# Performance work log

Hardware: AMD Instinct MI355X
Metric: run time of the kernel (lower is better)

The kernel has to match this reference:

```python
import jax, jax.numpy as jnp
import numpy as np

B, D, F, H = 4096, 1024, 1024, 8


def setup_inputs() -> dict:
    key = jax.random.key(0)
    k1, k2, k3, k4 = jax.random.split(key, 4)
    inputs = jax.random.normal(k1, (B, D), dtype=jnp.float32)
    indices = jax.random.randint(k2, (B,), 0, H, dtype=jnp.int64)
    # lecun_normal-like scale for kernel; zeros bias per flax defaults, but use
    # small random bias so gradients are nontrivial
    kernel = jax.random.normal(k3, (H, D, F), dtype=jnp.float32) / np.sqrt(D)
    bias = jax.random.normal(k4, (H, F), dtype=jnp.float32) * 0.01
    return {"inputs": inputs, "indices": indices, "kernel": kernel, "bias": bias}


def reference(inputs, indices, kernel, bias):
    # Original: per-example gather of kernel[idx] ([D,F]) then x[idx] @ w + b.
    # Equivalent math, vectorized: compute all heads densely then select the
    # routed head per example (avoids materializing a [B,D,F] gathered tensor).
    y = jnp.einsum("bd,hdf->bhf", inputs, kernel) + bias[None, :, :]  # [B,H,F]
    return y[jnp.arange(inputs.shape[0]), indices]  # [B,F]
```

## Files before the change

kernel.cpp:

```cpp
#include <hip/hip_runtime.h>


typedef __attribute__((ext_vector_type(8))) short bf16x8;
typedef __attribute__((ext_vector_type(4))) float f32x4;

#define WAITV(N) asm volatile("s_waitcnt vmcnt(" #N ")" ::: "memory")

static __device__ __forceinline__ unsigned short f2bf(float f) {
  union { float f; unsigned int u; } c; c.f = f;
  unsigned int u = c.u;
  return (unsigned short)((u + 0x7fffu + ((u >> 16) & 1u)) >> 16);
}

static __device__ __forceinline__ void gload16(const void* g, void* s) {
  __builtin_amdgcn_global_load_lds(
      (const __attribute__((address_space(1))) void*)g,
      (__attribute__((address_space(3))) void*)s, 16, 0, 0);
}

__global__ __launch_bounds__(256) void k_prep(
    const float* __restrict__ W, const int* __restrict__ idx,
    unsigned short* __restrict__ Wt, int* __restrict__ cnt,
    int* __restrict__ base8, int* __restrict__ rows) {
  const int bid = blockIdx.x;
  const int t = threadIdx.x;

  if (bid >= 2048) {
    __shared__ int sc[256][8];
    int myi[16];
#pragma unroll
    for (int i = 0; i < 4; ++i) {
      const int4 v = *(const int4*)(idx + t * 16 + i * 4);
      myi[i * 4 + 0] = v.x; myi[i * 4 + 1] = v.y;
      myi[i * 4 + 2] = v.z; myi[i * 4 + 3] = v.w;
    }
    int c[8];
#pragma unroll
    for (int h = 0; h < 8; ++h) c[h] = 0;
#pragma unroll
    for (int e = 0; e < 16; ++e)
#pragma unroll
      for (int h = 0; h < 8; ++h) c[h] += (myi[e] == h) ? 1 : 0;

    int val[8];
#pragma unroll
    for (int h = 0; h < 8; ++h) { val[h] = c[h]; sc[t][h] = c[h]; }
    __syncthreads();
    for (int off = 1; off < 256; off <<= 1) {
      int nb[8];
#pragma unroll
      for (int h = 0; h < 8; ++h) nb[h] = (t >= off) ? sc[t - off][h] : 0;
      __syncthreads();
#pragma unroll
      for (int h = 0; h < 8; ++h) { val[h] += nb[h]; sc[t][h] = val[h]; }
      __syncthreads();
    }
    int tot[8], excl[8];
#pragma unroll
    for (int h = 0; h < 8; ++h) tot[h] = sc[255][h];
#pragma unroll
    for (int h = 0; h < 8; ++h) excl[h] = val[h] - c[h];
    int bases[9];
    bases[0] = 0;
#pragma unroll
    for (int h = 0; h < 7; ++h) bases[h + 1] = (bases[h] + tot[h] + 7) & ~7;
    bases[8] = bases[7] + tot[7];
#pragma unroll
    for (int h = 0; h < 8; ++h) {
      int pos = bases[h] + excl[h];
#pragma unroll
      for (int e = 0; e < 16; ++e) {
        if (myi[e] == h) { rows[pos] = t * 16 + e; ++pos; }
      }
    }
    if (t < 56) {
      const int hh = t >> 3, j = t & 7;
      const int pos = bases[hh] + tot[hh] + j;
      if (pos < bases[hh + 1]) rows[pos] = 0;
    }
    if (t < 128) {
      const int pos = bases[8] + t;
      if (pos < 4160) rows[pos] = 0;
    }
    if (t < 8) cnt[t] = tot[t];
    if (t == 0) {
#pragma unroll
      for (int h = 0; h < 9; ++h) base8[h] = bases[h];
    }
    return;
  }

  __shared__ unsigned short tile[64][68];
  const int h = bid >> 8;
  const int rem = bid & 255;
  const int d0 = (rem >> 4) << 6;
  const int f0 = (rem & 15) << 6;
  const int c4 = (t & 15) * 4;
  const int r0 = t >> 4;
#pragma unroll
  for (int i = 0; i < 4; ++i) {
    const int r = r0 + i * 16;
    const float4 v = *(const float4*)(W + (size_t)(h * 1024 + d0 + r) * 1024 + f0 + c4);
    tile[r][c4 + 0] = f2bf(v.x);
    tile[r][c4 + 1] = f2bf(v.y);
    tile[r][c4 + 2] = f2bf(v.z);
    tile[r][c4 + 3] = f2bf(v.w);
  }
  __syncthreads();
  const int chunk = c4 >> 3;
  const int half = (c4 >> 2) & 1;
#pragma unroll
  for (int i = 0; i < 4; ++i) {
    const int fr = r0 + i * 16;
    const int frow = f0 + fr;
    ushort4 o;
    o.x = tile[c4 + 0][fr];
    o.y = tile[c4 + 1][fr];
    o.z = tile[c4 + 2][fr];
    o.w = tile[c4 + 3][fr];
    const int cS = chunk ^ (frow & 7);
    *(ushort4*)((char*)Wt + (size_t)(h * 1024 + frow) * 2048 +
                (d0 << 1) + (cS << 4) + (half << 3)) = o;
  }
}

__global__ __launch_bounds__(256) void k_gather(
    const float* __restrict__ X, const int* __restrict__ rows,
    unsigned short* __restrict__ Ap) {
  const int slot = blockIdx.x;
  const int b = rows[slot];
  const int t = threadIdx.x;
  const float4 v = *(const float4*)(X + (size_t)b * 1024 + t * 4);
  ushort4 o;
  o.x = f2bf(v.x); o.y = f2bf(v.y); o.z = f2bf(v.z); o.w = f2bf(v.w);
  const int g = t >> 4;
  const int cS = ((t >> 1) & 7) ^ (slot & 7);
  *(ushort4*)((char*)Ap + (size_t)slot * 2048 + (g << 7) + (cS << 4) +
              ((t & 1) << 3)) = o;
}

__global__ __launch_bounds__(256) void k_gemm(
    const unsigned short* __restrict__ Ap, const unsigned short* __restrict__ Wt,
    const int* __restrict__ rows, const int* __restrict__ cnt,
    const int* __restrict__ base8,
    const float* __restrict__ bias, float* __restrict__ out) {
  __shared__ __align__(16) unsigned short As[3][64 * 64];
  __shared__ __align__(16) unsigned short Bs[3][64 * 64];

  const int blk = blockIdx.x;
  const int h = blk & 7;
  const int nt = (blk >> 3) & 15;
  const int mt = blk >> 7;

  const int cnt_h = cnt[h];
  const int basep = base8[h];
  const int m0 = mt * 64;
  if (m0 >= cnt_h) return;
  const int n0 = nt * 64;

  const int t = threadIdx.x;
  const int lane = t & 63;
  const int wave = t >> 6;
  const int wr = wave >> 1, wc = wave & 1;

  const int srow = t >> 3;
  const int scol = (t & 7) << 4;
  int ar0 = basep + m0 + srow;      ar0 = ar0 < 4159 ? ar0 : 4159;
  int ar1 = basep + m0 + 32 + srow; ar1 = ar1 < 4159 ? ar1 : 4159;
  const char* aRow0 = (const char*)Ap + (size_t)ar0 * 2048 + scol;
  const char* aRow1 = (const char*)Ap + (size_t)ar1 * 2048 + scol;
  const char* bRow0 = (const char*)Wt + (size_t)(h * 1024 + n0 + srow) * 2048 + scol;
  const char* bRow1 = (const char*)Wt + (size_t)(h * 1024 + n0 + 32 + srow) * 2048 + scol;

  f32x4 acc[2][2];
#pragma unroll
  for (int m = 0; m < 2; ++m)
#pragma unroll
    for (int n = 0; n < 2; ++n)
      acc[m][n] = (f32x4){0.f, 0.f, 0.f, 0.f};

  auto stage = [&](char* aDst, char* bDst, int k0) {
    const int kby = k0 * 2;
    gload16(aRow0 + kby, aDst + t * 16);
    gload16(aRow1 + kby, aDst + 4096 + t * 16);
    gload16(bRow0 + kby, bDst + t * 16);
    gload16(bRow1 + kby, bDst + 4096 + t * 16);
  };

  const int swz = (lane & 7) << 4;
  const int ra = (wr * 32 + (lane & 15)) * 128;
  const int rb = (wc * 32 + (lane & 15)) * 128;
  const int kc = (lane >> 4) << 4;

  auto compute = [&](const char* ab, const char* bb) {
#pragma unroll
    for (int ksub = 0; ksub < 2; ++ksub) {
      const int co = ((ksub * 64) + kc) ^ swz;
      const bf16x8 a0 = *(const bf16x8*)(ab + ra + co);
      const bf16x8 a1 = *(const bf16x8*)(ab + ra + 2048 + co);
      const bf16x8 b0 = *(const bf16x8*)(bb + rb + co);
      const bf16x8 b1 = *(const bf16x8*)(bb + rb + 2048 + co);
      acc[0][0] = __builtin_amdgcn_mfma_f32_16x16x32_bf16(a0, b0, acc[0][0], 0, 0, 0);
      acc[0][1] = __builtin_amdgcn_mfma_f32_16x16x32_bf16(a0, b1, acc[0][1], 0, 0, 0);
      acc[1][0] = __builtin_amdgcn_mfma_f32_16x16x32_bf16(a1, b0, acc[1][0], 0, 0, 0);
      acc[1][1] = __builtin_amdgcn_mfma_f32_16x16x32_bf16(a1, b1, acc[1][1], 0, 0, 0);
    }
  };

  char* a0p = (char*)&As[0][0]; char* a1p = (char*)&As[1][0]; char* a2p = (char*)&As[2][0];
  char* b0p = (char*)&Bs[0][0]; char* b1p = (char*)&Bs[1][0]; char* b2p = (char*)&Bs[2][0];

  stage(a0p, b0p, 0);
  stage(a1p, b1p, 64);

  for (int ts = 0; ts < 15; ++ts) {
    WAITV(4);
    __builtin_amdgcn_s_barrier();
    __builtin_amdgcn_sched_barrier(0);
    if (ts < 14) stage(a2p, b2p, (ts + 2) * 64);
    __builtin_amdgcn_sched_barrier(0);
    compute(a0p, b0p);
    char* tA = a0p; a0p = a1p; a1p = a2p; a2p = tA;
    char* tB = b0p; b0p = b1p; b1p = b2p; b2p = tB;
  }
  WAITV(0);
  __builtin_amdgcn_s_barrier();
  __builtin_amdgcn_sched_barrier(0);
  compute(a0p, b0p);

  int rmap[2][4];
  bool vld[2][4];
#pragma unroll
  for (int m = 0; m < 2; ++m) {
#pragma unroll
    for (int j = 0; j < 4; ++j) {
      const int lr = wr * 32 + m * 16 + (lane >> 4) * 4 + j;
      const bool v = (m0 + lr) < cnt_h;
      vld[m][j] = v;
      rmap[m][j] = v ? rows[basep + m0 + lr] : 0;
    }
  }
#pragma unroll
  for (int n = 0; n < 2; ++n) {
    const int c = n0 + wc * 32 + n * 16 + (lane & 15);
    const float bv = bias[h * 1024 + c];
#pragma unroll
    for (int m = 0; m < 2; ++m) {
#pragma unroll
      for (int j = 0; j < 4; ++j) {
        if (vld[m][j])
          out[(size_t)rmap[m][j] * 1024 + c] = acc[m][n][j] + bv;
      }
    }
  }
}

extern "C" void kernel_launch(void* const* d_in, const int* in_sizes, int n_in,
                              void* d_out, int out_size, void* d_ws, size_t ws_size,
                              hipStream_t stream) {
  const float* X = (const float*)d_in[0];
  const int* idx = (const int*)d_in[1];
  const float* W = (const float*)d_in[2];
  const float* bias = (const float*)d_in[3];
  float* out = (float*)d_out;

  char* ws = (char*)d_ws;
  int* cnt = (int*)ws;
  int* base8 = (int*)(ws + 64);
  int* rows = (int*)(ws + 256);
  unsigned short* Wt = (unsigned short*)(ws + 32768);
  unsigned short* Ap = (unsigned short*)(ws + 32768 + 16777216);

  k_prep<<<dim3(2049), 256, 0, stream>>>(W, idx, Wt, cnt, base8, rows);
  k_gather<<<dim3(4160), 256, 0, stream>>>(X, rows, Ap);
  k_gemm<<<dim3(8 * 16 * 16), 256, 0, stream>>>(Ap, Wt, rows, cnt, base8, bias, out);
}
```

Before: 48.90 us.

## Pre-pack weights in MFMA fragment order and load B directly to registers

The prep kernel now writes the bf16 weights in a fragment-major layout, so each lane of a wave can load its MFMA B operand with one contiguous 16-byte global load. The GEMM stops staging B through LDS: it register-double-buffers B and keeps only a double-buffered A tile in shared memory. The goal is to cut LDS traffic and footprint and shorten the pipeline. The cost is higher register pressure and less latency hiding, since B now waits on a direct global load each step. Head segments are padded to 16 rows, which enlarges the gather grid and the zero-fill of the row list.

```diff
diff --git a/kernel.cpp b/kernel.cpp
--- a/kernel.cpp
+++ b/kernel.cpp
@@ -21,7 +21,7 @@
 __global__ __launch_bounds__(256) void k_prep(
     const float* __restrict__ W, const int* __restrict__ idx,
     unsigned short* __restrict__ Wt, int* __restrict__ cnt,
-    int* __restrict__ base8, int* __restrict__ rows) {
+    int* __restrict__ base16, int* __restrict__ rows) {
   const int bid = blockIdx.x;
   const int t = threadIdx.x;
 
@@ -63,7 +63,7 @@
     int bases[9];
     bases[0] = 0;
 #pragma unroll
-    for (int h = 0; h < 7; ++h) bases[h + 1] = (bases[h] + tot[h] + 7) & ~7;
+    for (int h = 0; h < 7; ++h) bases[h + 1] = (bases[h] + tot[h] + 15) & ~15;
     bases[8] = bases[7] + tot[7];
 #pragma unroll
     for (int h = 0; h < 8; ++h) {
@@ -73,54 +73,61 @@
         if (myi[e] == h) { rows[pos] = t * 16 + e; ++pos; }
       }
     }
-    if (t < 56) {
-      const int hh = t >> 3, j = t & 7;
+    if (t < 128) {
+      const int hh = t >> 4, j = t & 15;
       const int pos = bases[hh] + tot[hh] + j;
       if (pos < bases[hh + 1]) rows[pos] = 0;
     }
-    if (t < 128) {
+    {
       const int pos = bases[8] + t;
-      if (pos < 4160) rows[pos] = 0;
+      if (pos < 4352) rows[pos] = 0;
     }
     if (t < 8) cnt[t] = tot[t];
     if (t == 0) {
 #pragma unroll
-      for (int h = 0; h < 9; ++h) base8[h] = bases[h];
+      for (int h = 0; h < 9; ++h) base16[h] = bases[h];
     }
     return;
   }
 
-  __shared__ unsigned short tile[64][68];
+  __shared__ unsigned short tile[64][65];
   const int h = bid >> 8;
   const int rem = bid & 255;
   const int d0 = (rem >> 4) << 6;
   const int f0 = (rem & 15) << 6;
-  const int c4 = (t & 15) * 4;
-  const int r0 = t >> 4;
-#pragma unroll
-  for (int i = 0; i < 4; ++i) {
-    const int r = r0 + i * 16;
-    const float4 v = *(const float4*)(W + (size_t)(h * 1024 + d0 + r) * 1024 + f0 + c4);
-    tile[r][c4 + 0] = f2bf(v.x);
-    tile[r][c4 + 1] = f2bf(v.y);
-    tile[r][c4 + 2] = f2bf(v.z);
-    tile[r][c4 + 3] = f2bf(v.w);
+  {
+    const int c4 = (t & 15) * 4;
+    const int r0 = t >> 4;
+#pragma unroll
+    for (int i = 0; i < 4; ++i) {
+      const int r = r0 + i * 16;
+      const float4 v = *(const float4*)(W + (size_t)(h * 1024 + d0 + r) * 1024 + f0 + c4);
+      tile[r][c4 + 0] = f2bf(v.x);
+      tile[r][c4 + 1] = f2bf(v.y);
+      tile[r][c4 + 2] = f2bf(v.z);
+      tile[r][c4 + 3] = f2bf(v.w);
+    }
   }
   __syncthreads();
-  const int chunk = c4 >> 3;
-  const int half = (c4 >> 2) & 1;
-#pragma unroll
-  for (int i = 0; i < 4; ++i) {
-    const int fr = r0 + i * 16;
-    const int frow = f0 + fr;
+  const int fgl = t >> 6;
+  const int fr = t & 15;
+  const int ksl = (t >> 4) & 3;
+  const int frow = f0 + fgl * 16 + fr;
+  const int fg = frow >> 4;
+  const int kc = (d0 >> 5) + (ksl >> 1);
+  const int kg0 = (ksl & 1) * 2;
+  const size_t baseB = (((size_t)(h * 64 + fg) * 32) + kc) * 1024;
+#pragma unroll
+  for (int q = 0; q < 4; ++q) {
+    const int kg = kg0 + (q >> 1);
+    const int e = (q & 1) * 4;
+    const int dl = ksl * 16 + (q >> 1) * 8 + e;
     ushort4 o;
-    o.x = tile[c4 + 0][fr];
-    o.y = tile[c4 + 1][fr];
-    o.z = tile[c4 + 2][fr];
-    o.w = tile[c4 + 3][fr];
-    const int cS = chunk ^ (frow & 7);
-    *(ushort4*)((char*)Wt + (size_t)(h * 1024 + frow) * 2048 +
-                (d0 << 1) + (cS << 4) + (half << 3)) = o;
+    o.x = tile[dl + 0][fgl * 16 + fr];
+    o.y = tile[dl + 1][fgl * 16 + fr];
+    o.z = tile[dl + 2][fgl * 16 + fr];
+    o.w = tile[dl + 3][fgl * 16 + fr];
+    *(ushort4*)((char*)Wt + baseB + kg * 256 + fr * 16 + e * 2) = o;
   }
 }
 
@@ -142,10 +149,10 @@
 __global__ __launch_bounds__(256) void k_gemm(
     const unsigned short* __restrict__ Ap, const unsigned short* __restrict__ Wt,
     const int* __restrict__ rows, const int* __restrict__ cnt,
-    const int* __restrict__ base8,
+    const int* __restrict__ base16,
     const float* __restrict__ bias, float* __restrict__ out) {
-  __shared__ __align__(16) unsigned short As[3][64 * 64];
-  __shared__ __align__(16) unsigned short Bs[3][64 * 64];
+  __shared__ __align__(16) unsigned short As0[64 * 64];
+  __shared__ __align__(16) unsigned short As1[64 * 64];
 
   const int blk = blockIdx.x;
   const int h = blk & 7;
@@ -153,7 +160,7 @@
   const int mt = blk >> 7;
 
   const int cnt_h = cnt[h];
-  const int basep = base8[h];
+  const int basep = base16[h];
   const int m0 = mt * 64;
   if (m0 >= cnt_h) return;
   const int n0 = nt * 64;
@@ -165,94 +172,111 @@
 
   const int srow = t >> 3;
   const int scol = (t & 7) << 4;
-  int ar0 = basep + m0 + srow;      ar0 = ar0 < 4159 ? ar0 : 4159;
-  int ar1 = basep + m0 + 32 + srow; ar1 = ar1 < 4159 ? ar1 : 4159;
+  int ar0 = basep + m0 + srow;      ar0 = ar0 < 4351 ? ar0 : 4351;
+  int ar1 = basep + m0 + 32 + srow; ar1 = ar1 < 4351 ? ar1 : 4351;
   const char* aRow0 = (const char*)Ap + (size_t)ar0 * 2048 + scol;
   const char* aRow1 = (const char*)Ap + (size_t)ar1 * 2048 + scol;
-  const char* bRow0 = (const char*)Wt + (size_t)(h * 1024 + n0 + srow) * 2048 + scol;
-  const char* bRow1 = (const char*)Wt + (size_t)(h * 1024 + n0 + 32 + srow) * 2048 + scol;
-
-  f32x4 acc[2][2];
-#pragma unroll
-  for (int m = 0; m < 2; ++m)
-#pragma unroll
-    for (int n = 0; n < 2; ++n)
-      acc[m][n] = (f32x4){0.f, 0.f, 0.f, 0.f};
-
-  auto stage = [&](char* aDst, char* bDst, int k0) {
-    const int kby = k0 * 2;
-    gload16(aRow0 + kby, aDst + t * 16);
-    gload16(aRow1 + kby, aDst + 4096 + t * 16);
-    gload16(bRow0 + kby, bDst + t * 16);
-    gload16(bRow1 + kby, bDst + 4096 + t * 16);
-  };
+
+#define STAGEA(DST, ts_) do {                                   \
+    const int kby_ = (ts_) * 128;                               \
+    gload16(aRow0 + kby_, (char*)(DST) + t * 16);               \
+    gload16(aRow1 + kby_, (char*)(DST) + 4096 + t * 16);        \
+  } while (0)
+
+  const int fg0 = nt * 4 + wc * 2;
+  const char* bBase0 = (const char*)Wt + (size_t)(h * 64 + fg0) * 32768 + lane * 16;
+  const char* bBase1 = (const char*)Wt + (size_t)(h * 64 + fg0 + 1) * 32768 + lane * 16;
+
+  bf16x8 c00, c01, c10, c11;
+  bf16x8 n00, n01, n10, n11;
+
+#define BLOAD(P00, P01, P10, P11, ts_) do {                     \
+    if ((ts_) < 16) {                                           \
+      const size_t kb_ = (size_t)(ts_) * 2048;                  \
+      P00 = *(const bf16x8*)(bBase0 + kb_);                     \
+      P01 = *(const bf16x8*)(bBase0 + kb_ + 1024);              \
+      P10 = *(const bf16x8*)(bBase1 + kb_);                     \
+      P11 = *(const bf16x8*)(bBase1 + kb_ + 1024);              \
+    }                                                           \
+  } while (0)
 
   const int swz = (lane & 7) << 4;
   const int ra = (wr * 32 + (lane & 15)) * 128;
-  const int rb = (wc * 32 + (lane & 15)) * 128;
   const int kc = (lane >> 4) << 4;
 
-  auto compute = [&](const char* ab, const char* bb) {
-#pragma unroll
-    for (int ksub = 0; ksub < 2; ++ksub) {
-      const int co = ((ksub * 64) + kc) ^ swz;
-      const bf16x8 a0 = *(const bf16x8*)(ab + ra + co);
-      const bf16x8 a1 = *(const bf16x8*)(ab + ra + 2048 + co);
-      const bf16x8 b0 = *(const bf16x8*)(bb + rb + co);
-      const bf16x8 b1 = *(const bf16x8*)(bb + rb + 2048 + co);
-      acc[0][0] = __builtin_amdgcn_mfma_f32_16x16x32_bf16(a0, b0, acc[0][0], 0, 0, 0);
-      acc[0][1] = __builtin_amdgcn_mfma_f32_16x16x32_bf16(a0, b1, acc[0][1], 0, 0, 0);
-      acc[1][0] = __builtin_amdgcn_mfma_f32_16x16x32_bf16(a1, b0, acc[1][0], 0, 0, 0);
-      acc[1][1] = __builtin_amdgcn_mfma_f32_16x16x32_bf16(a1, b1, acc[1][1], 0, 0, 0);
-    }
-  };
-
-  char* a0p = (char*)&As[0][0]; char* a1p = (char*)&As[1][0]; char* a2p = (char*)&As[2][0];
-  char* b0p = (char*)&Bs[0][0]; char* b1p = (char*)&Bs[1][0]; char* b2p = (char*)&Bs[2][0];
-
-  stage(a0p, b0p, 0);
-  stage(a1p, b1p, 64);
-
-  for (int ts = 0; ts < 15; ++ts) {
+  f32x4 acc00 = {0.f, 0.f, 0.f, 0.f}, acc01 = {0.f, 0.f, 0.f, 0.f};
+  f32x4 acc10 = {0.f, 0.f, 0.f, 0.f}, acc11 = {0.f, 0.f, 0.f, 0.f};
+
+#define COMPUTE(ABUF, B00, B01, B10, B11) do {                                   \
+    const char* ab_ = (const char*)(ABUF);                                       \
+    {                                                                            \
+      const int co_ = kc ^ swz;                                                  \
+      const bf16x8 a0_ = *(const bf16x8*)(ab_ + ra + co_);                       \
+      const bf16x8 a1_ = *(const bf16x8*)(ab_ + ra + 2048 + co_);                \
+      acc00 = __builtin_amdgcn_mfma_f32_16x16x32_bf16(a0_, B00, acc00, 0, 0, 0); \
+      acc01 = __builtin_amdgcn_mfma_f32_16x16x32_bf16(a0_, B10, acc01, 0, 0, 0); \
+      acc10 = __builtin_amdgcn_mfma_f32_16x16x32_bf16(a1_, B00, acc10, 0, 0, 0); \
+      acc11 = __builtin_amdgcn_mfma_f32_16x16x32_bf16(a1_, B10, acc11, 0, 0, 0); \
+    }                                                                            \
+    {                                                                            \
+      const int co_ = (64 + kc) ^ swz;                                           \
+      const bf16x8 a0_ = *(const bf16x8*)(ab_ + ra + co_);                       \
+      const bf16x8 a1_ = *(const bf16x8*)(ab_ + ra + 2048 + co_);                \
+      acc00 = __builtin_amdgcn_mfma_f32_16x16x32_bf16(a0_, B01, acc00, 0, 0, 0); \
+      acc01 = __builtin_amdgcn_mfma_f32_16x16x32_bf16(a0_, B11, acc01, 0, 0, 0); \
+      acc10 = __builtin_amdgcn_mfma_f32_16x16x32_bf16(a1_, B01, acc10, 0, 0, 0); \
+      acc11 = __builtin_amdgcn_mfma_f32_16x16x32_bf16(a1_, B11, acc11, 0, 0, 0); \
+    }                                                                            \
+  } while (0)
+
+  STAGEA(As0, 0);
+  BLOAD(c00, c01, c10, c11, 0);
+  WAITV(4);
+  __builtin_amdgcn_s_barrier();
+  __builtin_amdgcn_sched_barrier(0);
+
+#pragma unroll 1
+  for (int it = 0; it < 8; ++it) {
+    const int ts = it * 2;
+    if (ts + 1 < 16) STAGEA(As1, ts + 1);
+    BLOAD(n00, n01, n10, n11, ts + 1);
+    COMPUTE(As0, c00, c01, c10, c11);
     WAITV(4);
     __builtin_amdgcn_s_barrier();
     __builtin_amdgcn_sched_barrier(0);
-    if (ts < 14) stage(a2p, b2p, (ts + 2) * 64);
+    if (ts + 2 < 16) STAGEA(As0, ts + 2);
+    BLOAD(c00, c01, c10, c11, ts + 2);
+    COMPUTE(As1, n00, n01, n10, n11);
+    WAITV(4);
+    __builtin_amdgcn_s_barrier();
     __builtin_amdgcn_sched_barrier(0);
-    compute(a0p, b0p);
-    char* tA = a0p; a0p = a1p; a1p = a2p; a2p = tA;
-    char* tB = b0p; b0p = b1p; b1p = b2p; b2p = tB;
-  }
-  WAITV(0);
-  __builtin_amdgcn_s_barrier();
-  __builtin_amdgcn_sched_barrier(0);
-  compute(a0p, b0p);
-
-  int rmap[2][4];
-  bool vld[2][4];
+  }
+
+  const int jrow = (lane >> 4) * 4;
+  const int ccol = lane & 15;
 #pragma unroll
   for (int m = 0; m < 2; ++m) {
 #pragma unroll
     for (int j = 0; j < 4; ++j) {
-      const int lr = wr * 32 + m * 16 + (lane >> 4) * 4 + j;
-      const bool v = (m0 + lr) < cnt_h;
-      vld[m][j] = v;
-      rmap[m][j] = v ? rows[basep + m0 + lr] : 0;
-    }
-  }
-#pragma unroll
-  for (int n = 0; n < 2; ++n) {
-    const int c = n0 + wc * 32 + n * 16 + (lane & 15);
-    const float bv = bias[h * 1024 + c];
-#pragma unroll
-    for (int m = 0; m < 2; ++m) {
-#pragma unroll
-      for (int j = 0; j < 4; ++j) {
-        if (vld[m][j])
-          out[(size_t)rmap[m][j] * 1024 + c] = acc[m][n][j] + bv;
+      const int lr = wr * 32 + m * 16 + jrow + j;
+      if (m0 + lr < cnt_h) {
+        const int b = rows[basep + m0 + lr];
+#pragma unroll
+        for (int n = 0; n < 2; ++n) {
+          const int c = n0 + wc * 32 + n * 16 + ccol;
+          float v;
+          if (m == 0 && n == 0) v = acc00[j];
+          else if (m == 0 && n == 1) v = acc01[j];
+          else if (m == 1 && n == 0) v = acc10[j];
+          else v = acc11[j];
+          out[(size_t)b * 1024 + c] = v + bias[h * 1024 + c];
+        }
       }
     }
   }
+#undef STAGEA
+#undef BLOAD
+#undef COMPUTE
 }
 
 extern "C" void kernel_launch(void* const* d_in, const int* in_sizes, int n_in,
@@ -266,12 +290,12 @@
 
   char* ws = (char*)d_ws;
   int* cnt = (int*)ws;
-  int* base8 = (int*)(ws + 64);
+  int* base16 = (int*)(ws + 64);
   int* rows = (int*)(ws + 256);
   unsigned short* Wt = (unsigned short*)(ws + 32768);
   unsigned short* Ap = (unsigned short*)(ws + 32768 + 16777216);
 
-  k_prep<<<dim3(2049), 256, 0, stream>>>(W, idx, Wt, cnt, base8, rows);
-  k_gather<<<dim3(4160), 256, 0, stream>>>(X, rows, Ap);
-  k_gemm<<<dim3(8 * 16 * 16), 256, 0, stream>>>(Ap, Wt, rows, cnt, base8, bias, out);
-}
+  k_prep<<<dim3(2049), 256, 0, stream>>>(W, idx, Wt, cnt, base16, rows);
+  k_gather<<<dim3(4352), 256, 0, stream>>>(X, rows, Ap);
+  k_gemm<<<dim3(8 * 16 * 16), 256, 0, stream>>>(Ap, Wt, rows, cnt, base16, bias, out);
+}
```

New measurement: 47.35 us. 1.03x faster.
